# Kernel optimization log

Hardware: AMD Instinct MI355X
Metric: run time of the kernel (lower is better)

The kernel has to match this reference:

```python
import jax, jax.numpy as jnp
import numpy as np

E = 8      # num_experts
A = 128    # angle feature size = input_size - 4
TGT = 3    # target size
HID = 16   # expert MLP hidden / latent / main GRU hidden
OUT = 128  # motion decoder output size
B = 64
W = 128
F = A + TGT + 1  # 132
BN_EPS = 1e-5


def _gru_layer(x, Wih, Whh, bih, bhh):
    # x: (B, T, I); Wih: (3H, I); Whh: (3H, H). PyTorch GRU equations.
    xW = jnp.einsum('bti,gi->btg', x, Wih) + bih  # precompute input gates (B,T,3H)
    H = Whh.shape[1]

    def step(h, xw):
        gh = h @ Whh.T + bhh
        ir, iz, inn = jnp.split(xw, 3, axis=-1)
        hr, hz, hn = jnp.split(gh, 3, axis=-1)
        r = jax.nn.sigmoid(ir + hr)
        z = jax.nn.sigmoid(iz + hz)
        n = jnp.tanh(inn + r * hn)
        h_new = (1.0 - z) * n + z * h
        return h_new, h_new

    h0 = jnp.zeros((x.shape[0], H), x.dtype)
    _, ys = jax.lax.scan(step, h0, jnp.swapaxes(xW, 0, 1))
    return jnp.swapaxes(ys, 0, 1)  # (B, T, H)


def _expert_mlp(x, om, w1, b1, w2, b2, g, bt):
    # Blend expert weights per-sample, then matvec; fused as one einsum (same math).
    h = jnp.einsum('bi,be,eih->bh', x, om, w1) + om @ b1
    # BatchNorm1d, training-mode batch statistics (biased variance), then ELU
    m = h.mean(0)
    v = h.var(0)
    h = jax.nn.elu(g * (h - m) * jax.lax.rsqrt(v + BN_EPS) + bt)
    return jnp.einsum('bh,be,eho->bo', h, om, w2) + om @ b2


def _forward(Local, Remote,
             gW_ih0, gW_hh0, gb_ih0, gb_hh0, gW_ih1, gW_hh1, gb_ih1, gb_hh1,
             ae_w1, ae_b1, ae_w2, ae_b2, ae_g, ae_bt,
             md_w1, md_b1, md_w2, md_b2, md_g, md_bt,
             mW_ih0, mW_hh0, mb_ih0, mb_hh0, mW_ih1, mW_hh1, mb_ih1, mb_hh1):
    Bn, Wn, _ = Local.shape
    LA = Local[..., :A]
    RA = Remote[..., :A]
    LT = Local[..., A:A + TGT]
    RT = Remote[..., A:A + TGT]
    Scale = Remote[..., A + TGT]  # (B, W)

    def gate(t):
        h = _gru_layer(t, gW_ih0, gW_hh0, gb_ih0, gb_hh0)
        h = _gru_layer(h, gW_ih1, gW_hh1, gb_ih1, gb_hh1)
        return jax.nn.softmax(h, axis=-1)

    Lo = gate(LT)  # (B, W, E)
    Ro = gate(RT)

    ZL = _expert_mlp(LA.reshape(-1, A), Lo.reshape(-1, E), ae_w1, ae_b1, ae_w2, ae_b2, ae_g, ae_bt)
    ZR = _expert_mlp(RA.reshape(-1, A), Ro.reshape(-1, E), ae_w1, ae_b1, ae_w2, ae_b2, ae_g, ae_bt)
    Z = (ZL + ZR).reshape(Bn, Wn, HID)

    Z = _gru_layer(Z, mW_ih0, mW_hh0, mb_ih0, mb_hh0)
    Z = _gru_layer(Z, mW_ih1, mW_hh1, mb_ih1, mb_hh1)
    Z = Z[:, -1]  # (B, HID)

    dec_in = jnp.concatenate([Z, Scale[:, -1:]], axis=-1)  # (B, HID+1)
    return _expert_mlp(dec_in, Ro[:, -1], md_w1, md_b1, md_w2, md_b2, md_g, md_bt)


def setup_inputs() -> dict:
    key = jax.random.key(0)
    ks = iter(jax.random.split(key, 40))

    def u(shape, bound):
        return jax.random.uniform(next(ks), shape, jnp.float32, -bound, bound)

    d = {}
    d['Local'] = jax.random.normal(next(ks), (B, W, F), jnp.float32)
    d['Remote'] = jax.random.normal(next(ks), (B, W, F), jnp.float32)

    def gru_params(pref, isz, hsz):
        bd = 1.0 / np.sqrt(hsz)
        d[pref + 'W_ih0'] = u((3 * hsz, isz), bd)
        d[pref + 'W_hh0'] = u((3 * hsz, hsz), bd)
        d[pref + 'b_ih0'] = u((3 * hsz,), bd)
        d[pref + 'b_hh0'] = u((3 * hsz,), bd)
        d[pref + 'W_ih1'] = u((3 * hsz, hsz), bd)
        d[pref + 'W_hh1'] = u((3 * hsz, hsz), bd)
        d[pref + 'b_ih1'] = u((3 * hsz,), bd)
        d[pref + 'b_hh1'] = u((3 * hsz,), bd)

    gru_params('g', TGT, E)    # gating GRU: 2 layers, hidden = num_experts
    gru_params('m', HID, HID)  # main GRU: 2 layers, hidden = 16

    def expert(pref, isz, hsz, osz):
        b1 = float(np.sqrt(6.0 / (isz * hsz)))
        b2 = float(np.sqrt(6.0 / (hsz * osz)))
        d[pref + '_w1'] = u((E, isz, hsz), b1)
        d[pref + '_b1'] = jnp.zeros((E, hsz), jnp.float32)
        d[pref + '_w2'] = u((E, hsz, osz), b2)
        d[pref + '_b2'] = jnp.zeros((E, osz), jnp.float32)
        d[pref + '_g'] = jnp.ones((hsz,), jnp.float32)
        d[pref + '_bt'] = jnp.zeros((hsz,), jnp.float32)

    expert('ae', A, HID, HID)        # angle encoder
    expert('md', HID + 1, HID, OUT)  # motion decoder
    return d


def reference(Local, Remote,
              gW_ih0, gW_hh0, gb_ih0, gb_hh0, gW_ih1, gW_hh1, gb_ih1, gb_hh1,
              ae_w1, ae_b1, ae_w2, ae_b2, ae_g, ae_bt,
              md_w1, md_b1, md_w2, md_b2, md_g, md_bt,
              mW_ih0, mW_hh0, mb_ih0, mb_hh0, mW_ih1, mW_hh1, mb_ih1, mb_hh1):
    return _forward(Local, Remote,
                    gW_ih0, gW_hh0, gb_ih0, gb_hh0, gW_ih1, gW_hh1, gb_ih1, gb_hh1,
                    ae_w1, ae_b1, ae_w2, ae_b2, ae_g, ae_bt,
                    md_w1, md_b1, md_w2, md_b2, md_g, md_bt,
                    mW_ih0, mW_hh0, mb_ih0, mb_hh0, mW_ih1, mW_hh1, mb_ih1, mb_hh1)
```

## Files before the change

### kernel.cpp

```cpp
#include <hip/hip_runtime.h>
#include <cstdint>
#include <cstddef>

#define DEV __device__ __forceinline__

typedef float v16f __attribute__((ext_vector_type(16)));

DEV float fsig(float x)  { return __builtin_amdgcn_rcpf(1.0f + __expf(-x)); }
DEV float ftanh_(float x){ return 1.0f - 2.0f * __builtin_amdgcn_rcpf(1.0f + __expf(2.0f * x)); }
DEV float readlanef(float v, int l) {
    return __uint_as_float(__builtin_amdgcn_readlane(__float_as_uint(v), l));
}

constexpr size_t ACC   = 0;
constexpr size_t LO    = 128;
constexpr size_t RO    = LO + 65536;
constexpr size_t HBUF  = RO + 65536;
constexpr size_t ZLAST = HBUF + 262144;

__global__ __launch_bounds__(64, 1) void k1_gate(
    const float* __restrict__ Local, const float* __restrict__ Remote,
    const float* __restrict__ Wih0, const float* __restrict__ Whh0,
    const float* __restrict__ bih0, const float* __restrict__ bhh0,
    const float* __restrict__ Wih1, const float* __restrict__ Whh1,
    const float* __restrict__ bih1, const float* __restrict__ bhh1,
    float* __restrict__ ws)
{
    const int tid = threadIdx.x;
    const int j = tid & 7;
    const int layer = (tid >> 3) & 1;
    const int blk = blockIdx.x;
    const int track = blk >> 6;
    const int b = blk & 63;
    if (blk == 0) ws[ACC + tid] = 0.f;

    __shared__ float xwg[128][24];
    __shared__ float h1all[128][9];

    const float* __restrict__ src = track ? Remote : Local;
    for (int t = tid; t < 128; t += 64) {
        const float* p = src + ((size_t)b * 128 + t) * 132 + 128;
        float x0 = p[0], x1 = p[1], x2 = p[2];
#pragma unroll
        for (int u = 0; u < 24; ++u) {
            float a = bih0[u];
            a = fmaf(Wih0[u * 3 + 0], x0, a);
            a = fmaf(Wih0[u * 3 + 1], x1, a);
            a = fmaf(Wih0[u * 3 + 2], x2, a);
            xwg[t][u] = a;
        }
    }

    const float* __restrict__ Wlo = layer ? Wih1 : Whh0;
    const float mhi = layer ? 1.f : 0.f;
    const float m0f = layer ? 0.f : 1.f;
    v16f wr, wz, wc;
#pragma unroll
    for (int k = 0; k < 8; ++k) {
        wr[k] = Wlo[j * 8 + k];
        wz[k] = Wlo[(8 + j) * 8 + k];
        wc[k] = Wlo[(16 + j) * 8 + k];
        wr[8 + k] = mhi * Whh1[j * 8 + k];
        wz[8 + k] = mhi * Whh1[(8 + j) * 8 + k];
        wc[8 + k] = mhi * Whh1[(16 + j) * 8 + k];
    }
    const float base_r  = layer ? (bih1[j] + bhh1[j])         : bhh0[j];
    const float base_z  = layer ? (bih1[8 + j] + bhh1[8 + j]) : bhh0[8 + j];
    const float base_in = layer ? bih1[16 + j]                : 0.f;
    const float base_dn = layer ? bhh1[16 + j]                : bhh0[16 + j];
    __syncthreads();

    float hown = 0.f;
    float p0 = xwg[0][j], p1 = xwg[0][8 + j], p2 = xwg[0][16 + j];
#pragma unroll 1
    for (int t = 0; t <= 128; ++t) {
        int tn = t < 127 ? t + 1 : 127;
        float q0 = xwg[tn][j], q1 = xwg[tn][8 + j], q2 = xwg[tn][16 + j];
        float ar_a = fmaf(m0f, p0, base_r), ar_b = 0.f;
        float az_a = fmaf(m0f, p1, base_z), az_b = 0.f;
        float ac_lo = 0.f, ac_hi = 0.f;
#pragma unroll
        for (int k = 0; k < 8; ++k) {
            float blo = readlanef(hown, k);
            float bhi = readlanef(hown, 8 + k);
            ar_a  = fmaf(wr[k], blo, ar_a);
            az_a  = fmaf(wz[k], blo, az_a);
            ac_lo = fmaf(wc[k], blo, ac_lo);
            ar_b  = fmaf(wr[8 + k], bhi, ar_b);
            az_b  = fmaf(wz[8 + k], bhi, az_b);
            ac_hi = fmaf(wc[8 + k], bhi, ac_hi);
        }
        float r = fsig(ar_a + ar_b);
        float z = fsig(az_a + az_b);
        float tin = base_in + ac_lo;
        float in_ = layer ? tin : p2;
        float dn  = base_dn + (layer ? ac_hi : ac_lo);
        float n = ftanh_(in_ + r * dn);
        float hnew = (1.f - z) * n + z * hown;
        bool act = layer ? (t >= 1) : (t < 128);
        hown = act ? hnew : hown;
        if (tid >= 8 && tid < 16 && t >= 1) h1all[t - 1][j] = hown;
        p0 = q0; p1 = q1; p2 = q2;
    }
    __syncthreads();

    float* __restrict__ outp = ws + (track ? RO : LO);
    for (int t = tid; t < 128; t += 64) {
        float vv[8];
#pragma unroll
        for (int k = 0; k < 8; ++k) vv[k] = h1all[t][k];
        float mx = vv[0];
#pragma unroll
        for (int k = 1; k < 8; ++k) mx = fmaxf(mx, vv[k]);
        float ssum = 0.f;
#pragma unroll
        for (int k = 0; k < 8; ++k) { vv[k] = __expf(vv[k] - mx); ssum += vv[k]; }
        float inv = __builtin_amdgcn_rcpf(ssum);
        size_t base = ((size_t)b * 128 + t) * 8;
        float4 o0 = make_float4(vv[0] * inv, vv[1] * inv, vv[2] * inv, vv[3] * inv);
        float4 o1 = make_float4(vv[4] * inv, vv[5] * inv, vv[6] * inv, vv[7] * inv);
        *(float4*)(outp + base) = o0;
        *(float4*)(outp + base + 4) = o1;
    }
}

__global__ __launch_bounds__(256) void k2_expert1(
    const float* __restrict__ Local, const float* __restrict__ Remote,
    const float* __restrict__ ae_w1, const float* __restrict__ ae_b1,
    float* __restrict__ ws)
{
    const int blk = blockIdx.x;
    const int track = blk >> 7;
    const int n0 = (blk & 127) * 64;
    const float* __restrict__ X = track ? Remote : Local;
    const float* __restrict__ om = ws + (track ? RO : LO);

    __shared__ __align__(16) float xsh[64 * 132];
    __shared__ __align__(16) float wsh[16 * 1040];
    __shared__ float omsh[64][8];
    __shared__ float b1sh[128];
    __shared__ float red[32];
    const int tid = threadIdx.x;

    for (int i = tid; i < 2048; i += 256) {
        int r = i >> 5, q = i & 31;
        ((float4*)&xsh[r * 132])[q] = ((const float4*)(X + (size_t)(n0 + r) * 132))[q];
    }
    for (int i4 = tid; i4 < 4096; i4 += 256) {
        float4 v = ((const float4*)ae_w1)[i4];
        int i = i4 * 4;
#pragma unroll
        for (int c = 0; c < 4; ++c) {
            int ii = i + c;
            int h = ii & 15, kk = (ii >> 4) & 127, e = ii >> 11;
            float vc = c == 0 ? v.x : c == 1 ? v.y : c == 2 ? v.z : v.w;
            wsh[h * 1040 + e * 130 + kk] = vc;
        }
    }
    for (int i = tid; i < 512; i += 256) omsh[i >> 3][i & 7] = om[(size_t)(n0 + (i >> 3)) * 8 + (i & 7)];
    for (int i = tid; i < 128; i += 256) b1sh[i] = ae_b1[i];
    if (tid < 32) red[tid] = 0.f;
    __syncthreads();

    const int hh = tid & 15, rg = tid >> 4;
    float acc[4][8];
#pragma unroll
    for (int r = 0; r < 4; ++r)
#pragma unroll
        for (int e = 0; e < 8; ++e) acc[r][e] = 0.f;

#pragma unroll 4
    for (int kq = 0; kq < 32; ++kq) {
        float4 xv[4], wv[8];
#pragma unroll
        for (int r = 0; r < 4; ++r) xv[r] = *(const float4*)&xsh[(rg * 4 + r) * 132 + kq * 4];
#pragma unroll
        for (int e = 0; e < 8; ++e) wv[e] = *(const float4*)&wsh[hh * 1040 + e * 130 + kq * 4];
#pragma unroll
        for (int r = 0; r < 4; ++r)
#pragma unroll
            for (int e = 0; e < 8; ++e) {
                float a = acc[r][e];
                a = fmaf(xv[r].x, wv[e].x, a);
                a = fmaf(xv[r].y, wv[e].y, a);
                a = fmaf(xv[r].z, wv[e].z, a);
                a = fmaf(xv[r].w, wv[e].w, a);
                acc[r][e] = a;
            }
    }

    float s = 0.f, s2 = 0.f;
    float* __restrict__ hout = ws + HBUF + (size_t)track * 131072;
#pragma unroll
    for (int r = 0; r < 4; ++r) {
        int row = rg * 4 + r;
        float hv = 0.f;
#pragma unroll
        for (int e = 0; e < 8; ++e) hv = fmaf(omsh[row][e], acc[r][e] + b1sh[e * 16 + hh], hv);
        hout[(size_t)(n0 + row) * 16 + hh] = hv;
        s += hv; s2 += hv * hv;
    }
    __syncthreads();
    atomicAdd(&red[hh], s);
    atomicAdd(&red[16 + hh], s2);
    __syncthreads();
    if (tid < 32) atomicAdd(&ws[ACC + track * 32 + tid], red[tid]);
}

__global__ __launch_bounds__(256, 1) void k34_fused(
    const float* __restrict__ ae_w2, const float* __restrict__ ae_b2,
    const float* __restrict__ ae_g, const float* __restrict__ ae_bt,
    const float* __restrict__ mWih0, const float* __restrict__ mbih0,
    const float* __restrict__ Whh0, const float* __restrict__ bhh0,
    const float* __restrict__ Wih1, const float* __restrict__ Whh1,
    const float* __restrict__ bih1, const float* __restrict__ bhh1,
    float* __restrict__ ws)
{
    const int s = blockIdx.x;
    const int tid = threadIdx.x;

    __shared__ float stat[4][16];
    __shared__ float omsh[2][128][8];
    __shared__ float w2sh[2048];
    __shared__ float b2sh[128];
    __shared__ float actsh[2][128][16];
    __shared__ float zsh[128][17];
    __shared__ float wihsh[48][17];
    __shared__ float bihsh[48];
    __shared__ float xwsh[128 * 48];

    if (tid < 32) {
        int trk = tid >> 4, h = tid & 15;
        float sm = ws[ACC + trk * 32 + h], s2 = ws[ACC + trk * 32 + 16 + h];
        float m = sm * (1.f / 8192.f);
        float v = fmaxf(s2 * (1.f / 8192.f) - m * m, 0.f);
        stat[trk * 2][h] = m;
        stat[trk * 2 + 1][h] = rsqrtf(v + 1e-5f);
    }
    for (int i = tid; i < 2048; i += 256) w2sh[i] = ae_w2[i];
    for (int i = tid; i < 128; i += 256) b2sh[i] = ae_b2[i];
    for (int i = tid; i < 768; i += 256) wihsh[i >> 4][i & 15] = mWih0[i];
    if (tid < 48) bihsh[tid] = mbih0[tid];
    for (int i = tid; i < 2048; i += 256) {
        int trk = i >> 10, r = (i >> 3) & 127, e = i & 7;
        omsh[trk][r][e] = ws[(trk ? RO : LO) + ((size_t)s * 128 + r) * 8 + e];
    }
    __syncthreads();

    for (int i = tid; i < 4096; i += 256) {
        int trk = i >> 11, r = (i >> 4) & 127, h = i & 15;
        float v = ws[HBUF + (size_t)trk * 131072 + ((size_t)s * 128 + r) * 16 + h];
        float a = ae_g[h] * (v - stat[trk * 2][h]) * stat[trk * 2 + 1][h] + ae_bt[h];
        actsh[trk][r][h] = a > 0.f ? a : expm1f(a);
    }
    __syncthreads();

    for (int i = tid; i < 2048; i += 256) {
        int r = i >> 4, o = i & 15;
        float accv = 0.f;
#pragma unroll
        for (int trk = 0; trk < 2; ++trk) {
#pragma unroll
            for (int e = 0; e < 8; ++e) {
                const float* w = &w2sh[e * 256 + o];
                float t = b2sh[e * 16 + o];
#pragma unroll
                for (int h = 0; h < 16; ++h) t = fmaf(actsh[trk][r][h], w[h * 16], t);
                accv = fmaf(omsh[trk][r][e], t, accv);
            }
        }
        zsh[r][o] = accv;
    }
    __syncthreads();

    for (int i = tid; i < 6144; i += 256) {
        int r = i / 48, g = i - r * 48;
        float a = bihsh[g];
#pragma unroll
        for (int k = 0; k < 16; ++k) a = fmaf(zsh[r][k], wihsh[g][k], a);
        xwsh[r * 48 + g] = a;
    }
    __syncthreads();

    if (tid >= 64) return;

    const int j = tid & 15;
    const int layer = (tid >> 4) & 1;

    const float* __restrict__ Wlo = layer ? Wih1 : Whh0;
    const float mhi = layer ? 1.f : 0.f;
    const float m0f = layer ? 0.f : 1.f;
    v16f wr0, wr1, wz0, wz1, wc0, wc1;
#pragma unroll
    for (int k = 0; k < 16; ++k) {
        wr0[k] = Wlo[j * 16 + k];
        wz0[k] = Wlo[(16 + j) * 16 + k];
        wc0[k] = Wlo[(32 + j) * 16 + k];
        wr1[k] = mhi * Whh1[j * 16 + k];
        wz1[k] = mhi * Whh1[(16 + j) * 16 + k];
        wc1[k] = mhi * Whh1[(32 + j) * 16 + k];
    }
    const float base_r  = layer ? (bih1[j] + bhh1[j])           : bhh0[j];
    const float base_z  = layer ? (bih1[16 + j] + bhh1[16 + j]) : bhh0[16 + j];
    const float base_in = layer ? bih1[32 + j]                  : 0.f;
    const float base_dn = layer ? bhh1[32 + j]                  : bhh0[32 + j];

    float hown = 0.f;
    float p0 = xwsh[j], p1 = xwsh[16 + j], p2 = xwsh[32 + j];
#pragma unroll 1
    for (int t = 0; t <= 128; ++t) {
        int tn = (t < 127 ? t + 1 : 127) * 48;
        float q0 = xwsh[tn + j], q1 = xwsh[tn + 16 + j], q2 = xwsh[tn + 32 + j];
        float ar_a = fmaf(m0f, p0, base_r), ar_b = 0.f;
        float az_a = fmaf(m0f, p1, base_z), az_b = 0.f;
        float ac_lo = 0.f, ac_hi = 0.f;
#pragma unroll
        for (int k = 0; k < 16; ++k) {
            float blo = readlanef(hown, k);
            float bhi = readlanef(hown, 16 + k);
            ar_a  = fmaf(wr0[k], blo, ar_a);
            az_a  = fmaf(wz0[k], blo, az_a);
            ac_lo = fmaf(wc0[k], blo, ac_lo);
            ar_b  = fmaf(wr1[k], bhi, ar_b);
            az_b  = fmaf(wz1[k], bhi, az_b);
            ac_hi = fmaf(wc1[k], bhi, ac_hi);
        }
        float r = fsig(ar_a + ar_b);
        float z = fsig(az_a + az_b);
        float tin = base_in + ac_lo;
        float in_ = layer ? tin : p2;
        float dn  = base_dn + (layer ? ac_hi : ac_lo);
        float n = ftanh_(in_ + r * dn);
        float hnew = (1.f - z) * n + z * hown;
        bool act = layer ? (t >= 1) : (t < 128);
        hown = act ? hnew : hown;
        p0 = q0; p1 = q1; p2 = q2;
    }
    if (tid >= 16 && tid < 32) ws[ZLAST + (size_t)s * 16 + j] = hown;
}

__global__ __launch_bounds__(256) void k5_dec(
    const float* __restrict__ Remote,
    const float* __restrict__ md_w1, const float* __restrict__ md_b1,
    const float* __restrict__ md_g, const float* __restrict__ md_bt,
    const float* __restrict__ md_w2, const float* __restrict__ md_b2,
    const float* __restrict__ ws, float* __restrict__ out)
{
    const int o0 = blockIdx.x * 8;
    const int tid = threadIdx.x;
    __shared__ float xsh[64][17];
    __shared__ float omsh[64][8];
    __shared__ float w1sh[2176];
    __shared__ float b1sh[128];
    __shared__ float hsh[64][17];
    __shared__ float ssum[16], ss2[16], mstat[2][16];
    __shared__ float ash[64][17];
    __shared__ float w2sh[8][16][8];
    __shared__ float b2sh[8][8];

    for (int i = tid; i < 1024; i += 256) xsh[i >> 4][i & 15] = ws[ZLAST + i];
    if (tid < 64) xsh[tid][16] = Remote[((size_t)tid * 128 + 127) * 132 + 131];
    for (int i = tid; i < 512; i += 256)
        omsh[i >> 3][i & 7] = ws[RO + ((size_t)(i >> 3) * 128 + 127) * 8 + (i & 7)];
    for (int i = tid; i < 2176; i += 256) w1sh[i] = md_w1[i];
    for (int i = tid; i < 128; i += 256) b1sh[i] = md_b1[i];
    for (int i = tid; i < 1024; i += 256) {
        int e = i >> 7, h = (i >> 3) & 15, oo = i & 7;
        w2sh[e][h][oo] = md_w2[((size_t)e * 16 + h) * 128 + o0 + oo];
    }
    if (tid < 64) b2sh[tid >> 3][tid & 7] = md_b2[(size_t)(tid >> 3) * 128 + o0 + (tid & 7)];
    if (tid < 16) { ssum[tid] = 0.f; ss2[tid] = 0.f; }
    __syncthreads();

    for (int i = tid; i < 1024; i += 256) {
        int b = i >> 4, h = i & 15;
        float accv = 0.f;
#pragma unroll
        for (int e = 0; e < 8; ++e) {
            float t = b1sh[e * 16 + h];
            const float* w = &w1sh[e * 272 + h];
#pragma unroll
            for (int i2 = 0; i2 < 17; ++i2) t = fmaf(xsh[b][i2], w[i2 * 16], t);
            accv = fmaf(omsh[b][e], t, accv);
        }
        hsh[b][h] = accv;
        atomicAdd(&ssum[h], accv);
        atomicAdd(&ss2[h], accv * accv);
    }
    __syncthreads();
    if (tid < 16) {
        float m = ssum[tid] * (1.f / 64.f);
        float v = fmaxf(ss2[tid] * (1.f / 64.f) - m * m, 0.f);
        mstat[0][tid] = m;
        mstat[1][tid] = rsqrtf(v + 1e-5f);
    }
    __syncthreads();
    for (int i = tid; i < 1024; i += 256) {
        int b = i >> 4, h = i & 15;
        float a = md_g[h] * (hsh[b][h] - mstat[0][h]) * mstat[1][h] + md_bt[h];
        ash[b][h] = a > 0.f ? a : expm1f(a);
    }
    __syncthreads();

    for (int i = tid; i < 512; i += 256) {
        int b = i >> 3, oo = i & 7;
        float accv = 0.f;
#pragma unroll
        for (int e = 0; e < 8; ++e) {
            float t = b2sh[e][oo];
#pragma unroll
            for (int h = 0; h < 16; ++h) t = fmaf(ash[b][h], w2sh[e][h][oo], t);
            accv = fmaf(omsh[b][e], t, accv);
        }
        out[(size_t)b * 128 + o0 + oo] = accv;
    }
}

extern "C" void kernel_launch(void* const* d_in, const int* in_sizes, int n_in,
                              void* d_out, int out_size, void* d_ws, size_t ws_size,
                              hipStream_t stream) {
    const float* Local  = (const float*)d_in[0];
    const float* Remote = (const float*)d_in[1];
    const float* gWih0  = (const float*)d_in[2];
    const float* gWhh0  = (const float*)d_in[3];
    const float* gbih0  = (const float*)d_in[4];
    const float* gbhh0  = (const float*)d_in[5];
    const float* gWih1  = (const float*)d_in[6];
    const float* gWhh1  = (const float*)d_in[7];
    const float* gbih1  = (const float*)d_in[8];
    const float* gbhh1  = (const float*)d_in[9];
    const float* mWih0  = (const float*)d_in[10];
    const float* mWhh0  = (const float*)d_in[11];
    const float* mbih0  = (const float*)d_in[12];
    const float* mbhh0  = (const float*)d_in[13];
    const float* mWih1  = (const float*)d_in[14];
    const float* mWhh1  = (const float*)d_in[15];
    const float* mbih1  = (const float*)d_in[16];
    const float* mbhh1  = (const float*)d_in[17];
    const float* ae_w1  = (const float*)d_in[18];
    const float* ae_b1  = (const float*)d_in[19];
    const float* ae_w2  = (const float*)d_in[20];
    const float* ae_b2  = (const float*)d_in[21];
    const float* ae_g   = (const float*)d_in[22];
    const float* ae_bt  = (const float*)d_in[23];
    const float* md_w1  = (const float*)d_in[24];
    const float* md_b1  = (const float*)d_in[25];
    const float* md_w2  = (const float*)d_in[26];
    const float* md_b2  = (const float*)d_in[27];
    const float* md_g   = (const float*)d_in[28];
    const float* md_bt  = (const float*)d_in[29];
    float* ws  = (float*)d_ws;
    float* out = (float*)d_out;

    k1_gate<<<128, 64, 0, stream>>>(Local, Remote, gWih0, gWhh0, gbih0, gbhh0,
                                    gWih1, gWhh1, gbih1, gbhh1, ws);
    k2_expert1<<<256, 256, 0, stream>>>(Local, Remote, ae_w1, ae_b1, ws);
    k34_fused<<<64, 256, 0, stream>>>(ae_w2, ae_b2, ae_g, ae_bt, mWih0, mbih0,
                                      mWhh0, mbhh0, mWih1, mWhh1, mbih1, mbhh1, ws);
    k5_dec<<<16, 256, 0, stream>>>(Remote, md_w1, md_b1, md_g, md_bt,
                                   md_w2, md_b2, ws, out);
}
```

Measured before the change: 250.1 us.

## Split GRU recurrence dot products across lane halves with swizzle reduction

Both wavefront-level two-layer GRU recurrences (gate GRU and main GRU) now split each hidden unit's 2H-wide dot product across two lane groups (k-halves). Each lane does half the FMAs and the partial sums are combined with a ds_swizzle xor exchange. The goal is to shorten the serial per-step critical path and cut per-lane weight registers. In exchange each step adds swizzle latency, and both readlane sources are still issued before a select, so the readlane count stays the same.

```diff
diff --git a/kernel.cpp b/kernel.cpp
--- a/kernel.cpp
+++ b/kernel.cpp
@@ -5,11 +5,18 @@
 #define DEV __device__ __forceinline__
 
 typedef float v16f __attribute__((ext_vector_type(16)));
+typedef float v8f  __attribute__((ext_vector_type(8)));
 
 DEV float fsig(float x)  { return __builtin_amdgcn_rcpf(1.0f + __expf(-x)); }
 DEV float ftanh_(float x){ return 1.0f - 2.0f * __builtin_amdgcn_rcpf(1.0f + __expf(2.0f * x)); }
 DEV float readlanef(float v, int l) {
     return __uint_as_float(__builtin_amdgcn_readlane(__float_as_uint(v), l));
+}
+DEV float swz16f(float v) {
+    return __uint_as_float(__builtin_amdgcn_ds_swizzle(__float_as_uint(v), 0x401F));
+}
+DEV float swz8f(float v) {
+    return __uint_as_float(__builtin_amdgcn_ds_swizzle(__float_as_uint(v), 0x201F));
 }
 
 constexpr size_t ACC   = 0;
@@ -28,7 +35,8 @@
 {
     const int tid = threadIdx.x;
     const int j = tid & 7;
-    const int layer = (tid >> 3) & 1;
+    const int khalf = (tid >> 3) & 1;
+    const int layer = (tid >> 4) & 1;
     const int blk = blockIdx.x;
     const int track = blk >> 6;
     const int b = blk & 63;
@@ -51,23 +59,21 @@
         }
     }
 
-    const float* __restrict__ Wlo = layer ? Wih1 : Whh0;
-    const float mhi = layer ? 1.f : 0.f;
-    const float m0f = layer ? 0.f : 1.f;
-    v16f wr, wz, wc;
+    const float* __restrict__ Wsel = layer ? (khalf ? Whh1 : Wih1) : Whh0;
+    const float kmask = (layer == 0 && khalf == 1) ? 0.f : 1.f;
+    v8f wr, wz, wc;
 #pragma unroll
     for (int k = 0; k < 8; ++k) {
-        wr[k] = Wlo[j * 8 + k];
-        wz[k] = Wlo[(8 + j) * 8 + k];
-        wc[k] = Wlo[(16 + j) * 8 + k];
-        wr[8 + k] = mhi * Whh1[j * 8 + k];
-        wz[8 + k] = mhi * Whh1[(8 + j) * 8 + k];
-        wc[8 + k] = mhi * Whh1[(16 + j) * 8 + k];
+        wr[k] = kmask * Wsel[j * 8 + k];
+        wz[k] = kmask * Wsel[(8 + j) * 8 + k];
+        wc[k] = kmask * Wsel[(16 + j) * 8 + k];
     }
     const float base_r  = layer ? (bih1[j] + bhh1[j])         : bhh0[j];
     const float base_z  = layer ? (bih1[8 + j] + bhh1[8 + j]) : bhh0[8 + j];
     const float base_in = layer ? bih1[16 + j]                : 0.f;
     const float base_dn = layer ? bhh1[16 + j]                : bhh0[16 + j];
+    const float m0f = layer ? 0.f : 1.f;
+    const bool khb = (khalf == 1);
     __syncthreads();
 
     float hown = 0.f;
@@ -76,30 +82,37 @@
     for (int t = 0; t <= 128; ++t) {
         int tn = t < 127 ? t + 1 : 127;
         float q0 = xwg[tn][j], q1 = xwg[tn][8 + j], q2 = xwg[tn][16 + j];
-        float ar_a = fmaf(m0f, p0, base_r), ar_b = 0.f;
-        float az_a = fmaf(m0f, p1, base_z), az_b = 0.f;
-        float ac_lo = 0.f, ac_hi = 0.f;
-#pragma unroll
-        for (int k = 0; k < 8; ++k) {
-            float blo = readlanef(hown, k);
-            float bhi = readlanef(hown, 8 + k);
-            ar_a  = fmaf(wr[k], blo, ar_a);
-            az_a  = fmaf(wz[k], blo, az_a);
-            ac_lo = fmaf(wc[k], blo, ac_lo);
-            ar_b  = fmaf(wr[8 + k], bhi, ar_b);
-            az_b  = fmaf(wz[8 + k], bhi, az_b);
-            ac_hi = fmaf(wc[8 + k], bhi, ac_hi);
-        }
-        float r = fsig(ar_a + ar_b);
-        float z = fsig(az_a + az_b);
-        float tin = base_in + ac_lo;
-        float in_ = layer ? tin : p2;
-        float dn  = base_dn + (layer ? ac_hi : ac_lo);
+        float pr0 = 0.f, pr1 = 0.f, pz0 = 0.f, pz1 = 0.f, pc0 = 0.f, pc1 = 0.f;
+#pragma unroll
+        for (int k = 0; k < 4; ++k) {
+            float sa0 = readlanef(hown, 2 * k);
+            float sa1 = readlanef(hown, 16 + 2 * k);
+            float va = khb ? sa1 : sa0;
+            float sb0 = readlanef(hown, 2 * k + 1);
+            float sb1 = readlanef(hown, 16 + 2 * k + 1);
+            float vb = khb ? sb1 : sb0;
+            pr0 = fmaf(wr[2 * k], va, pr0);
+            pz0 = fmaf(wz[2 * k], va, pz0);
+            pc0 = fmaf(wc[2 * k], va, pc0);
+            pr1 = fmaf(wr[2 * k + 1], vb, pr1);
+            pz1 = fmaf(wz[2 * k + 1], vb, pz1);
+            pc1 = fmaf(wc[2 * k + 1], vb, pc1);
+        }
+        float pr = pr0 + pr1, pz = pz0 + pz1, pc = pc0 + pc1;
+        float opr = swz8f(pr), opz = swz8f(pz), opc = swz8f(pc);
+        float ar = base_r + fmaf(m0f, p0, pr + opr);
+        float az = base_z + fmaf(m0f, p1, pz + opz);
+        float pc_k0 = khb ? opc : pc;
+        float pc_k1 = khb ? pc : opc;
+        float in_ = layer ? (base_in + pc_k0) : p2;
+        float dn  = base_dn + (layer ? pc_k1 : (pc + opc));
+        float r = fsig(ar);
+        float z = fsig(az);
         float n = ftanh_(in_ + r * dn);
         float hnew = (1.f - z) * n + z * hown;
         bool act = layer ? (t >= 1) : (t < 128);
         hown = act ? hnew : hown;
-        if (tid >= 8 && tid < 16 && t >= 1) h1all[t - 1][j] = hown;
+        if (tid >= 16 && tid < 24 && t >= 1) h1all[t - 1][j] = hown;
         p0 = q0; p1 = q1; p2 = q2;
     }
     __syncthreads();
@@ -285,25 +298,24 @@
     if (tid >= 64) return;
 
     const int j = tid & 15;
-    const int layer = (tid >> 4) & 1;
-
-    const float* __restrict__ Wlo = layer ? Wih1 : Whh0;
-    const float mhi = layer ? 1.f : 0.f;
-    const float m0f = layer ? 0.f : 1.f;
-    v16f wr0, wr1, wz0, wz1, wc0, wc1;
+    const int khalf = (tid >> 4) & 1;
+    const int layer = (tid >> 5) & 1;
+
+    const float* __restrict__ Wsel = layer ? (khalf ? Whh1 : Wih1) : Whh0;
+    const float kmask = (layer == 0 && khalf == 1) ? 0.f : 1.f;
+    v16f wr, wz, wc;
 #pragma unroll
     for (int k = 0; k < 16; ++k) {
-        wr0[k] = Wlo[j * 16 + k];
-        wz0[k] = Wlo[(16 + j) * 16 + k];
-        wc0[k] = Wlo[(32 + j) * 16 + k];
-        wr1[k] = mhi * Whh1[j * 16 + k];
-        wz1[k] = mhi * Whh1[(16 + j) * 16 + k];
-        wc1[k] = mhi * Whh1[(32 + j) * 16 + k];
+        wr[k] = kmask * Wsel[j * 16 + k];
+        wz[k] = kmask * Wsel[(16 + j) * 16 + k];
+        wc[k] = kmask * Wsel[(32 + j) * 16 + k];
     }
     const float base_r  = layer ? (bih1[j] + bhh1[j])           : bhh0[j];
     const float base_z  = layer ? (bih1[16 + j] + bhh1[16 + j]) : bhh0[16 + j];
     const float base_in = layer ? bih1[32 + j]                  : 0.f;
     const float base_dn = layer ? bhh1[32 + j]                  : bhh0[32 + j];
+    const float m0f = layer ? 0.f : 1.f;
+    const bool khb = (khalf == 1);
 
     float hown = 0.f;
     float p0 = xwsh[j], p1 = xwsh[16 + j], p2 = xwsh[32 + j];
@@ -311,32 +323,39 @@
     for (int t = 0; t <= 128; ++t) {
         int tn = (t < 127 ? t + 1 : 127) * 48;
         float q0 = xwsh[tn + j], q1 = xwsh[tn + 16 + j], q2 = xwsh[tn + 32 + j];
-        float ar_a = fmaf(m0f, p0, base_r), ar_b = 0.f;
-        float az_a = fmaf(m0f, p1, base_z), az_b = 0.f;
-        float ac_lo = 0.f, ac_hi = 0.f;
-#pragma unroll
-        for (int k = 0; k < 16; ++k) {
-            float blo = readlanef(hown, k);
-            float bhi = readlanef(hown, 16 + k);
-            ar_a  = fmaf(wr0[k], blo, ar_a);
-            az_a  = fmaf(wz0[k], blo, az_a);
-            ac_lo = fmaf(wc0[k], blo, ac_lo);
-            ar_b  = fmaf(wr1[k], bhi, ar_b);
-            az_b  = fmaf(wz1[k], bhi, az_b);
-            ac_hi = fmaf(wc1[k], bhi, ac_hi);
-        }
-        float r = fsig(ar_a + ar_b);
-        float z = fsig(az_a + az_b);
-        float tin = base_in + ac_lo;
-        float in_ = layer ? tin : p2;
-        float dn  = base_dn + (layer ? ac_hi : ac_lo);
+        float pr0 = 0.f, pr1 = 0.f, pz0 = 0.f, pz1 = 0.f, pc0 = 0.f, pc1 = 0.f;
+#pragma unroll
+        for (int k = 0; k < 8; ++k) {
+            float sa0 = readlanef(hown, 2 * k);
+            float sa1 = readlanef(hown, 32 + 2 * k);
+            float va = khb ? sa1 : sa0;
+            float sb0 = readlanef(hown, 2 * k + 1);
+            float sb1 = readlanef(hown, 32 + 2 * k + 1);
+            float vb = khb ? sb1 : sb0;
+            pr0 = fmaf(wr[2 * k], va, pr0);
+            pz0 = fmaf(wz[2 * k], va, pz0);
+            pc0 = fmaf(wc[2 * k], va, pc0);
+            pr1 = fmaf(wr[2 * k + 1], vb, pr1);
+            pz1 = fmaf(wz[2 * k + 1], vb, pz1);
+            pc1 = fmaf(wc[2 * k + 1], vb, pc1);
+        }
+        float pr = pr0 + pr1, pz = pz0 + pz1, pc = pc0 + pc1;
+        float opr = swz16f(pr), opz = swz16f(pz), opc = swz16f(pc);
+        float ar = base_r + fmaf(m0f, p0, pr + opr);
+        float az = base_z + fmaf(m0f, p1, pz + opz);
+        float pc_k0 = khb ? opc : pc;
+        float pc_k1 = khb ? pc : opc;
+        float in_ = layer ? (base_in + pc_k0) : p2;
+        float dn  = base_dn + (layer ? pc_k1 : (pc + opc));
+        float r = fsig(ar);
+        float z = fsig(az);
         float n = ftanh_(in_ + r * dn);
         float hnew = (1.f - z) * n + z * hown;
         bool act = layer ? (t >= 1) : (t < 128);
         hown = act ? hnew : hown;
         p0 = q0; p1 = q1; p2 = q2;
     }
-    if (tid >= 16 && tid < 32) ws[ZLAST + (size_t)s * 16 + j] = hown;
+    if (tid >= 32 && tid < 48) ws[ZLAST + (size_t)s * 16 + j] = hown;
 }
 
 __global__ __launch_bounds__(256) void k5_dec(
```

Measured after the change: 262.3 us. 1.05x slower.
